# Optimization experiments

Measured on AMD Instinct MI355X. Metric: run time of the kernel, lower is better.

Reference implementation:

```python
import jax, jax.numpy as jnp
import numpy as np

D_MODEL = 1024
N_HEADS = 16
D_HEAD = D_MODEL // N_HEADS


def setup_inputs() -> dict:
    key = jax.random.key(0)
    k1, k2, k3, k4, k5 = jax.random.split(key, 5)
    B, S = 2, 2048
    scale_in = 1.0 / np.sqrt(D_MODEL)
    return {
        "x": jax.random.normal(k1, (B, S, D_MODEL), dtype=jnp.float32),
        "qkv_w": jax.random.normal(k2, (3 * D_MODEL, D_MODEL), dtype=jnp.float32) * scale_in,
        "qkv_b": jax.random.normal(k3, (3 * D_MODEL,), dtype=jnp.float32) * 0.02,
        "out_w": jax.random.normal(k4, (D_MODEL, D_MODEL), dtype=jnp.float32) * scale_in,
        "out_b": jax.random.normal(k5, (D_MODEL,), dtype=jnp.float32) * 0.02,
    }


def reference(x, qkv_w, qkv_b, out_w, out_b) -> jnp.ndarray:
    B, S, D = x.shape
    # qkv projection: torch Linear stores weight as (out, in)
    qkv = x @ qkv_w.T + qkv_b                      # [B,S,3D]
    qkv = qkv.reshape(B, S, 3, N_HEADS, D_HEAD)
    qkv = jnp.transpose(qkv, (2, 0, 3, 1, 4))      # [3,B,H,S,d]
    q, k, v = qkv[0], qkv[1], qkv[2]
    scale = 1.0 / np.sqrt(D_HEAD).astype(np.float32)
    scores = jnp.einsum("bhsd,bhtd->bhst", q, k) * scale  # [B,H,S,S]
    attn = jax.nn.softmax(scores, axis=-1)
    out = jnp.einsum("bhst,bhtd->bhsd", attn, v)   # [B,H,S,d]
    out = jnp.transpose(out, (0, 2, 1, 3)).reshape(B, S, D)
    return out @ out_w.T + out_b
```

## Files before the change

kernel.cpp:

```cpp
#include <hip/hip_runtime.h>

typedef __bf16 bf16;
typedef __bf16 bf16x4 __attribute__((ext_vector_type(4)));
typedef __bf16 bf16x8 __attribute__((ext_vector_type(8)));
typedef float  f32x4  __attribute__((ext_vector_type(4)));

__device__ __forceinline__ void gld16(const void* g, void* l) {
  __builtin_amdgcn_global_load_lds(
      (const __attribute__((address_space(1))) void*)g,
      (__attribute__((address_space(3))) void*)l, 16, 0, 0);
}

__global__ void f2bf_all(const float* __restrict__ x, bf16* __restrict__ xo,
                         const float* __restrict__ w1, bf16* __restrict__ w1o,
                         const float* __restrict__ w2, bf16* __restrict__ w2o) {
  int i = blockIdx.x * blockDim.x + threadIdx.x;
  const float* in; bf16* out; int idx;
  if (i < 1048576)      { in = x;  out = xo;  idx = i; }
  else if (i < 1835008) { in = w1; out = w1o; idx = i - 1048576; }
  else                  { in = w2; out = w2o; idx = i - 1835008; }
  float4 v = reinterpret_cast<const float4*>(in)[idx];
  bf16x4 o = { (bf16)v.x, (bf16)v.y, (bf16)v.z, (bf16)v.w };
  reinterpret_cast<bf16x4*>(out)[idx] = o;
}

template<int MODE, int BN>
__global__ __launch_bounds__(256)
void gemm_bt(const bf16* __restrict__ A, const bf16* __restrict__ B,
             const float* __restrict__ bias, void* __restrict__ Cout,
             int K, int N) {
  __shared__ bf16 As[128 * 64];
  __shared__ bf16 Bs[BN * 64];
  const int tid  = threadIdx.x;
  const int wave = tid >> 6, lane = tid & 63;
  const int quad = lane >> 4, l16 = lane & 15;
  const int bm = blockIdx.x * 128, bn = blockIdx.y * BN;
  constexpr int NI  = (BN == 128) ? 4 : 2;
  constexpr int BCH = BN / 32;
  const int wr = (BN == 128) ? (wave >> 1) * 64 : wave * 32;
  const int wc = (BN == 128) ? (wave & 1) * 64 : 0;
  const int arow = lane >> 3;
  const int acol = (lane & 7) * 8;

  f32x4 acc[NI][4] = {};

  const bf16* Ab = A + (size_t)bm * K;
  const bf16* Bb = B + (size_t)bn * K;

  for (int k0 = 0; k0 < K; k0 += 64) {
#pragma unroll
    for (int i = 0; i < 4; ++i) {
      int c = wave * 4 + i;
      gld16(Ab + (size_t)(c * 8 + arow) * K + k0 + acol, As + c * 512);
    }
#pragma unroll
    for (int i = 0; i < BCH; ++i) {
      int c = wave * BCH + i;
      gld16(Bb + (size_t)(c * 8 + arow) * K + k0 + acol, Bs + c * 512);
    }
    __syncthreads();
#pragma unroll
    for (int kk = 0; kk < 64; kk += 32) {
      bf16x8 af[NI], bfr[4];
#pragma unroll
      for (int i = 0; i < NI; ++i)
        af[i]  = *(const bf16x8*)(As + (wr + i * 16 + l16) * 64 + kk + quad * 8);
#pragma unroll
      for (int j = 0; j < 4; ++j)
        bfr[j] = *(const bf16x8*)(Bs + (wc + j * 16 + l16) * 64 + kk + quad * 8);
#pragma unroll
      for (int i = 0; i < NI; ++i)
#pragma unroll
        for (int j = 0; j < 4; ++j)
          acc[i][j] = __builtin_amdgcn_mfma_f32_16x16x32_bf16(af[i], bfr[j], acc[i][j], 0, 0, 0);
    }
    __syncthreads();
  }

  if constexpr (MODE == 0) {
    bf16* Q = (bf16*)Cout;
#pragma unroll
    for (int j = 0; j < 4; ++j) {
      int col = bn + wc + j * 16 + l16;
      float bv  = bias[col];
      int sec = col >> 10, rem = col & 1023;
      int h = rem >> 6, d = rem & 63;
      float scl = (sec == 0) ? 0.125f * 1.44269504f : 1.0f;
#pragma unroll
      for (int i = 0; i < NI; ++i) {
#pragma unroll
        for (int r = 0; r < 4; ++r) {
          int row = bm + wr + i * 16 + quad * 4 + r;
          int b = row >> 11, si = row & 2047;
          float v = (acc[i][j][r] + bv) * scl;
          Q[(((size_t)sec * 32 + b * 16 + h) * 2048 + si) * 64 + d] = (bf16)v;
        }
      }
    }
  } else {
    float* C = (float*)Cout;
#pragma unroll
    for (int j = 0; j < 4; ++j) {
      int col = bn + wc + j * 16 + l16;
      float bv = bias[col];
#pragma unroll
      for (int i = 0; i < NI; ++i)
#pragma unroll
        for (int r = 0; r < 4; ++r) {
          int row = bm + wr + i * 16 + quad * 4 + r;
          C[(size_t)row * N + col] = acc[i][j][r] + bv;
        }
    }
  }
}

__global__ __launch_bounds__(256)
void transpose_v(const bf16* __restrict__ V, bf16* __restrict__ Vt) {
  __shared__ bf16 t[64][72];
  int bh = blockIdx.y, s0 = blockIdx.x * 64;
  const bf16* Vb = V + ((size_t)bh * 2048 + s0) * 64;
  bf16* Vtb = Vt + (size_t)bh * 64 * 2048 + s0;
  int tid = threadIdx.x;
#pragma unroll
  for (int p = 0; p < 2; ++p) {
    int r = p * 32 + (tid >> 3), c0 = (tid & 7) * 8;
    bf16x8 v = *(const bf16x8*)(Vb + r * 64 + c0);
#pragma unroll
    for (int j = 0; j < 8; ++j) t[c0 + j][r] = v[j];
  }
  __syncthreads();
#pragma unroll
  for (int p = 0; p < 2; ++p) {
    int d = p * 32 + (tid >> 3), s = (tid & 7) * 8;
    *(bf16x8*)(Vtb + (size_t)d * 2048 + s) = *(const bf16x8*)(&t[d][s]);
  }
}

__global__ __launch_bounds__(256, 2)
void attn_kernel(const bf16* __restrict__ QKV, const bf16* __restrict__ Vt,
                 bf16* __restrict__ O) {
  __shared__ bf16 Ks[2][128 * 72];
  __shared__ bf16 Ps[4][32 * 136];

  const int bh = blockIdx.y;
  const int q0 = blockIdx.x * 128;
  const bf16* Qg = QKV + ((size_t)bh * 2048 + q0) * 64;
  const bf16* Kg = QKV + (size_t)32 * 2048 * 64 + (size_t)bh * 2048 * 64;
  const bf16* Vg = Vt + (size_t)bh * 64 * 2048;

  const int tid  = threadIdx.x;
  const int wave = tid >> 6, lane = tid & 63;
  const int quad = lane >> 4, l16 = lane & 15;
  const int srow = tid >> 3;
  const int scol = (tid & 7) * 8;
  bf16* Pw = &Ps[wave][0];

  bf16x8 aq[2][2];
#pragma unroll
  for (int i = 0; i < 2; ++i)
#pragma unroll
    for (int kh = 0; kh < 2; ++kh)
      aq[i][kh] = *(const bf16x8*)(Qg + (size_t)(wave * 32 + i * 16 + l16) * 64 +
                                   kh * 32 + quad * 8);

  {
    bf16x8 kreg[4];
#pragma unroll
    for (int ch = 0; ch < 4; ++ch)
      kreg[ch] = *(const bf16x8*)(Kg + (size_t)(ch * 32 + srow) * 64 + scol);
#pragma unroll
    for (int ch = 0; ch < 4; ++ch)
      *(bf16x8*)(&Ks[0][(ch * 32 + srow) * 72 + scol]) = kreg[ch];
  }
  __syncthreads();

  float rs[2] = {0.f, 0.f};
  f32x4 o[2][4] = {};

  for (int kt = 0; kt < 16; ++kt) {
    const int cur = kt & 1;

    bf16x8 kreg[4];
    if (kt < 15) {
#pragma unroll
      for (int ch = 0; ch < 4; ++ch)
        kreg[ch] = *(const bf16x8*)(Kg + (size_t)((kt + 1) * 128 + ch * 32 + srow) * 64 + scol);
    }
    bf16x8 bv[4][4];
#pragma unroll
    for (int kk = 0; kk < 4; ++kk)
#pragma unroll
      for (int oj = 0; oj < 4; ++oj)
        bv[kk][oj] = *(const bf16x8*)(Vg + (size_t)(oj * 16 + l16) * 2048 +
                                      kt * 128 + kk * 32 + quad * 8);

    f32x4 s[2][8] = {};
#pragma unroll
    for (int kh = 0; kh < 2; ++kh) {
#pragma unroll
      for (int ni = 0; ni < 8; ++ni) {
        bf16x8 bk = *(const bf16x8*)(&Ks[cur][(ni * 16 + l16) * 72 + kh * 32 + quad * 8]);
        s[0][ni] = __builtin_amdgcn_mfma_f32_16x16x32_bf16(bk, aq[0][kh], s[0][ni], 0, 0, 0);
        s[1][ni] = __builtin_amdgcn_mfma_f32_16x16x32_bf16(bk, aq[1][kh], s[1][ni], 0, 0, 0);
      }
    }

    if (kt < 15) {
#pragma unroll
      for (int ch = 0; ch < 4; ++ch)
        *(bf16x8*)(&Ks[cur ^ 1][(ch * 32 + srow) * 72 + scol]) = kreg[ch];
    }

#pragma unroll
    for (int i = 0; i < 2; ++i)
#pragma unroll
      for (int ni = 0; ni < 8; ++ni) {
        float p0 = __builtin_amdgcn_exp2f(s[i][ni][0]);
        float p1 = __builtin_amdgcn_exp2f(s[i][ni][1]);
        float p2 = __builtin_amdgcn_exp2f(s[i][ni][2]);
        float p3 = __builtin_amdgcn_exp2f(s[i][ni][3]);
        rs[i] += (p0 + p1) + (p2 + p3);
        bf16x4 pk = { (bf16)p0, (bf16)p1, (bf16)p2, (bf16)p3 };
        *(bf16x4*)(Pw + (i * 16 + l16) * 136 + ni * 16 + quad * 4) = pk;
      }

#pragma unroll
    for (int kk = 0; kk < 4; ++kk) {
#pragma unroll
      for (int i = 0; i < 2; ++i) {
        bf16x8 ap = *(const bf16x8*)(Pw + (i * 16 + l16) * 136 + kk * 32 + quad * 8);
#pragma unroll
        for (int oj = 0; oj < 4; ++oj)
          o[i][oj] = __builtin_amdgcn_mfma_f32_16x16x32_bf16(ap, bv[kk][oj], o[i][oj], 0, 0, 0);
      }
    }

    __syncthreads();
  }

#pragma unroll
  for (int i = 0; i < 2; ++i) {
    rs[i] += __shfl_xor(rs[i], 16);
    rs[i] += __shfl_xor(rs[i], 32);
  }

  const int b = bh >> 4, h = bh & 15;
#pragma unroll
  for (int i = 0; i < 2; ++i)
#pragma unroll
    for (int r = 0; r < 4; ++r) {
      float lsum = __shfl(rs[i], quad * 4 + r);
      float inv = 1.0f / lsum;
      int row = q0 + wave * 32 + i * 16 + quad * 4 + r;
#pragma unroll
      for (int oj = 0; oj < 4; ++oj)
        O[((size_t)(b * 2048 + row)) * 1024 + h * 64 + oj * 16 + l16] =
            (bf16)(o[i][oj][r] * inv);
    }
}

extern "C" void kernel_launch(void* const* d_in, const int* in_sizes, int n_in,
                              void* d_out, int out_size, void* d_ws, size_t ws_size,
                              hipStream_t stream) {
  const float* x      = (const float*)d_in[0];
  const float* qkv_w  = (const float*)d_in[1];
  const float* qkv_b  = (const float*)d_in[2];
  const float* out_w  = (const float*)d_in[3];
  const float* out_b  = (const float*)d_in[4];
  float* out = (float*)d_out;

  char* ws = (char*)d_ws;
  bf16* Xb   = (bf16*)(ws);
  bf16* Wqkv = (bf16*)(ws + 8388608);
  bf16* Wout = (bf16*)(ws + 14680064);
  bf16* QKV  = (bf16*)(ws + 16777216);
  bf16* At   = (bf16*)(ws + 41943040);
  bf16* Vt   = Xb;

  f2bf_all<<<8192, 256, 0, stream>>>(x, Xb, qkv_w, Wqkv, out_w, Wout);

  gemm_bt<0, 128><<<dim3(32, 24), 256, 0, stream>>>(Xb, Wqkv, qkv_b, (void*)QKV, 1024, 3072);

  transpose_v<<<dim3(32, 32), 256, 0, stream>>>(QKV + (size_t)2 * 32 * 2048 * 64, Vt);

  attn_kernel<<<dim3(16, 32), 256, 0, stream>>>(QKV, Vt, At);

  gemm_bt<1, 64><<<dim3(32, 16), 256, 0, stream>>>(At, Wout, out_b, (void*)out, 1024, 1024);
}
```

Before: 228.1 us.

## Halve attention query tile to 64 rows and compute row sums via MFMA

Each attention block now handles 64 query rows (16 per wave) instead of 128, doubling the grid to 1024 blocks and raising the launch-bounds occupancy hint to 3. The softmax denominator is now accumulated with an extra MFMA against a vector of ones, which replaces the per-element VALU adds and the cross-lane shuffle reduction. This is meant to improve CU fill and reduce register pressure, at the cost of loading each K/V tile twice as often per query row. The row sum is now taken from the bf16-rounded probabilities, which slightly changes numerics.

After: 290.8 us. 1.27x slower.

```diff
diff --git a/kernel.cpp b/kernel.cpp
--- a/kernel.cpp
+++ b/kernel.cpp
@@ -136,14 +136,14 @@
   }
 }
 
-__global__ __launch_bounds__(256, 2)
+__global__ __launch_bounds__(256, 3)
 void attn_kernel(const bf16* __restrict__ QKV, const bf16* __restrict__ Vt,
                  bf16* __restrict__ O) {
   __shared__ bf16 Ks[2][128 * 72];
-  __shared__ bf16 Ps[4][32 * 136];
+  __shared__ bf16 Ps[4][16 * 136];
 
   const int bh = blockIdx.y;
-  const int q0 = blockIdx.x * 128;
+  const int q0 = blockIdx.x * 64;
   const bf16* Qg = QKV + ((size_t)bh * 2048 + q0) * 64;
   const bf16* Kg = QKV + (size_t)32 * 2048 * 64 + (size_t)bh * 2048 * 64;
   const bf16* Vg = Vt + (size_t)bh * 64 * 2048;
@@ -155,13 +155,10 @@
   const int scol = (tid & 7) * 8;
   bf16* Pw = &Ps[wave][0];
 
-  bf16x8 aq[2][2];
-#pragma unroll
-  for (int i = 0; i < 2; ++i)
-#pragma unroll
-    for (int kh = 0; kh < 2; ++kh)
-      aq[i][kh] = *(const bf16x8*)(Qg + (size_t)(wave * 32 + i * 16 + l16) * 64 +
-                                   kh * 32 + quad * 8);
+  bf16x8 aq[2];
+#pragma unroll
+  for (int kh = 0; kh < 2; ++kh)
+    aq[kh] = *(const bf16x8*)(Qg + (size_t)(wave * 16 + l16) * 64 + kh * 32 + quad * 8);
 
   {
     bf16x8 kreg[4];
@@ -174,8 +171,11 @@
   }
   __syncthreads();
 
-  float rs[2] = {0.f, 0.f};
-  f32x4 o[2][4] = {};
+  const bf16 one = (bf16)1.0f;
+  const bf16x8 bone = { one, one, one, one, one, one, one, one };
+
+  f32x4 o[4] = {};
+  f32x4 lacc = {};
 
   for (int kt = 0; kt < 16; ++kt) {
     const int cur = kt & 1;
@@ -194,14 +194,13 @@
         bv[kk][oj] = *(const bf16x8*)(Vg + (size_t)(oj * 16 + l16) * 2048 +
                                       kt * 128 + kk * 32 + quad * 8);
 
-    f32x4 s[2][8] = {};
+    f32x4 s[8] = {};
 #pragma unroll
     for (int kh = 0; kh < 2; ++kh) {
 #pragma unroll
       for (int ni = 0; ni < 8; ++ni) {
         bf16x8 bk = *(const bf16x8*)(&Ks[cur][(ni * 16 + l16) * 72 + kh * 32 + quad * 8]);
-        s[0][ni] = __builtin_amdgcn_mfma_f32_16x16x32_bf16(bk, aq[0][kh], s[0][ni], 0, 0, 0);
-        s[1][ni] = __builtin_amdgcn_mfma_f32_16x16x32_bf16(bk, aq[1][kh], s[1][ni], 0, 0, 0);
+        s[ni] = __builtin_amdgcn_mfma_f32_16x16x32_bf16(bk, aq[kh], s[ni], 0, 0, 0);
       }
     }
 
@@ -212,51 +211,37 @@
     }
 
 #pragma unroll
-    for (int i = 0; i < 2; ++i)
-#pragma unroll
-      for (int ni = 0; ni < 8; ++ni) {
-        float p0 = __builtin_amdgcn_exp2f(s[i][ni][0]);
-        float p1 = __builtin_amdgcn_exp2f(s[i][ni][1]);
-        float p2 = __builtin_amdgcn_exp2f(s[i][ni][2]);
-        float p3 = __builtin_amdgcn_exp2f(s[i][ni][3]);
-        rs[i] += (p0 + p1) + (p2 + p3);
-        bf16x4 pk = { (bf16)p0, (bf16)p1, (bf16)p2, (bf16)p3 };
-        *(bf16x4*)(Pw + (i * 16 + l16) * 136 + ni * 16 + quad * 4) = pk;
-      }
+    for (int ni = 0; ni < 8; ++ni) {
+      float p0 = __builtin_amdgcn_exp2f(s[ni][0]);
+      float p1 = __builtin_amdgcn_exp2f(s[ni][1]);
+      float p2 = __builtin_amdgcn_exp2f(s[ni][2]);
+      float p3 = __builtin_amdgcn_exp2f(s[ni][3]);
+      bf16x4 pk = { (bf16)p0, (bf16)p1, (bf16)p2, (bf16)p3 };
+      *(bf16x4*)(Pw + l16 * 136 + ni * 16 + quad * 4) = pk;
+    }
 
 #pragma unroll
     for (int kk = 0; kk < 4; ++kk) {
-#pragma unroll
-      for (int i = 0; i < 2; ++i) {
-        bf16x8 ap = *(const bf16x8*)(Pw + (i * 16 + l16) * 136 + kk * 32 + quad * 8);
-#pragma unroll
-        for (int oj = 0; oj < 4; ++oj)
-          o[i][oj] = __builtin_amdgcn_mfma_f32_16x16x32_bf16(ap, bv[kk][oj], o[i][oj], 0, 0, 0);
-      }
+      bf16x8 ap = *(const bf16x8*)(Pw + l16 * 136 + kk * 32 + quad * 8);
+      lacc = __builtin_amdgcn_mfma_f32_16x16x32_bf16(ap, bone, lacc, 0, 0, 0);
+#pragma unroll
+      for (int oj = 0; oj < 4; ++oj)
+        o[oj] = __builtin_amdgcn_mfma_f32_16x16x32_bf16(ap, bv[kk][oj], o[oj], 0, 0, 0);
     }
 
     __syncthreads();
   }
 
-#pragma unroll
-  for (int i = 0; i < 2; ++i) {
-    rs[i] += __shfl_xor(rs[i], 16);
-    rs[i] += __shfl_xor(rs[i], 32);
-  }
-
   const int b = bh >> 4, h = bh & 15;
 #pragma unroll
-  for (int i = 0; i < 2; ++i)
-#pragma unroll
-    for (int r = 0; r < 4; ++r) {
-      float lsum = __shfl(rs[i], quad * 4 + r);
-      float inv = 1.0f / lsum;
-      int row = q0 + wave * 32 + i * 16 + quad * 4 + r;
-#pragma unroll
-      for (int oj = 0; oj < 4; ++oj)
-        O[((size_t)(b * 2048 + row)) * 1024 + h * 64 + oj * 16 + l16] =
-            (bf16)(o[i][oj][r] * inv);
-    }
+  for (int r = 0; r < 4; ++r) {
+    float inv = 1.0f / lacc[r];
+    int row = q0 + wave * 16 + quad * 4 + r;
+#pragma unroll
+    for (int oj = 0; oj < 4; ++oj)
+      O[((size_t)(b * 2048 + row)) * 1024 + h * 64 + oj * 16 + l16] =
+          (bf16)(o[oj][r] * inv);
+  }
 }
 
 extern "C" void kernel_launch(void* const* d_in, const int* in_sizes, int n_in,
@@ -283,7 +268,7 @@
 
   transpose_v<<<dim3(32, 32), 256, 0, stream>>>(QKV + (size_t)2 * 32 * 2048 * 64, Vt);
 
-  attn_kernel<<<dim3(16, 32), 256, 0, stream>>>(QKV, Vt, At);
+  attn_kernel<<<dim3(32, 32), 256, 0, stream>>>(QKV, Vt, At);
 
   gemm_bt<1, 64><<<dim3(32, 16), 256, 0, stream>>>(At, Wout, out_b, (void*)out, 1024, 1024);
 }
```

## Fuse V transpose into QKV GEMM epilogue and reorder attention grid

Applied to the files above, without the earlier changes.

The QKV projection epilogue now writes the V section directly in transposed [bh][d][s] layout using packed 4-element bf16 stores, so the separate transpose_v kernel and its extra read/write pass are removed. The attention kernel now reads V^T from the QKV buffer region, and its grid is swapped so consecutive blocks cover different heads rather than consecutive query tiles of the same head. The V stores from the GEMM are strided by 2048 elements across lanes, which may be less coalesced than the original layout.

New measurement: 224.3 us. No clear change (-1.7%).

```diff
diff --git a/kernel.cpp b/kernel.cpp
--- a/kernel.cpp
+++ b/kernel.cpp
@@ -85,15 +85,27 @@
       float bv  = bias[col];
       int sec = col >> 10, rem = col & 1023;
       int h = rem >> 6, d = rem & 63;
-      float scl = (sec == 0) ? 0.125f * 1.44269504f : 1.0f;
-#pragma unroll
-      for (int i = 0; i < NI; ++i) {
-#pragma unroll
-        for (int r = 0; r < 4; ++r) {
-          int row = bm + wr + i * 16 + quad * 4 + r;
-          int b = row >> 11, si = row & 2047;
-          float v = (acc[i][j][r] + bv) * scl;
-          Q[(((size_t)sec * 32 + b * 16 + h) * 2048 + si) * 64 + d] = (bf16)v;
+      if (sec < 2) {
+        float scl = (sec == 0) ? 0.125f * 1.44269504f : 1.0f;
+#pragma unroll
+        for (int i = 0; i < NI; ++i) {
+#pragma unroll
+          for (int r = 0; r < 4; ++r) {
+            int row = bm + wr + i * 16 + quad * 4 + r;
+            int b = row >> 11, si = row & 2047;
+            float v = (acc[i][j][r] + bv) * scl;
+            Q[(((size_t)sec * 32 + b * 16 + h) * 2048 + si) * 64 + d] = (bf16)v;
+          }
+        }
+      } else {
+#pragma unroll
+        for (int i = 0; i < NI; ++i) {
+          int row0 = bm + wr + i * 16 + quad * 4;
+          int b = row0 >> 11, si = row0 & 2047;
+          bf16x4 pk = { (bf16)(acc[i][j][0] + bv), (bf16)(acc[i][j][1] + bv),
+                        (bf16)(acc[i][j][2] + bv), (bf16)(acc[i][j][3] + bv) };
+          *(bf16x4*)(Q + (size_t)2 * 4194304 +
+                     ((size_t)(b * 16 + h) * 64 + d) * 2048 + si) = pk;
         }
       }
     }
@@ -111,28 +123,6 @@
           C[(size_t)row * N + col] = acc[i][j][r] + bv;
         }
     }
-  }
-}
-
-__global__ __launch_bounds__(256)
-void transpose_v(const bf16* __restrict__ V, bf16* __restrict__ Vt) {
-  __shared__ bf16 t[64][72];
-  int bh = blockIdx.y, s0 = blockIdx.x * 64;
-  const bf16* Vb = V + ((size_t)bh * 2048 + s0) * 64;
-  bf16* Vtb = Vt + (size_t)bh * 64 * 2048 + s0;
-  int tid = threadIdx.x;
-#pragma unroll
-  for (int p = 0; p < 2; ++p) {
-    int r = p * 32 + (tid >> 3), c0 = (tid & 7) * 8;
-    bf16x8 v = *(const bf16x8*)(Vb + r * 64 + c0);
-#pragma unroll
-    for (int j = 0; j < 8; ++j) t[c0 + j][r] = v[j];
-  }
-  __syncthreads();
-#pragma unroll
-  for (int p = 0; p < 2; ++p) {
-    int d = p * 32 + (tid >> 3), s = (tid & 7) * 8;
-    *(bf16x8*)(Vtb + (size_t)d * 2048 + s) = *(const bf16x8*)(&t[d][s]);
   }
 }
 
@@ -142,8 +132,8 @@
   __shared__ bf16 Ks[2][128 * 72];
   __shared__ bf16 Ps[4][32 * 136];
 
-  const int bh = blockIdx.y;
-  const int q0 = blockIdx.x * 128;
+  const int bh = blockIdx.x;
+  const int q0 = blockIdx.y * 128;
   const bf16* Qg = QKV + ((size_t)bh * 2048 + q0) * 64;
   const bf16* Kg = QKV + (size_t)32 * 2048 * 64 + (size_t)bh * 2048 * 64;
   const bf16* Vg = Vt + (size_t)bh * 64 * 2048;
@@ -275,15 +265,13 @@
   bf16* Wout = (bf16*)(ws + 14680064);
   bf16* QKV  = (bf16*)(ws + 16777216);
   bf16* At   = (bf16*)(ws + 41943040);
-  bf16* Vt   = Xb;
+  bf16* VtP  = QKV + (size_t)2 * 32 * 2048 * 64;
 
   f2bf_all<<<8192, 256, 0, stream>>>(x, Xb, qkv_w, Wqkv, out_w, Wout);
 
   gemm_bt<0, 128><<<dim3(32, 24), 256, 0, stream>>>(Xb, Wqkv, qkv_b, (void*)QKV, 1024, 3072);
 
-  transpose_v<<<dim3(32, 32), 256, 0, stream>>>(QKV + (size_t)2 * 32 * 2048 * 64, Vt);
-
-  attn_kernel<<<dim3(16, 32), 256, 0, stream>>>(QKV, Vt, At);
+  attn_kernel<<<dim3(32, 16), 256, 0, stream>>>(QKV, VtP, At);
 
   gemm_bt<1, 64><<<dim3(32, 16), 256, 0, stream>>>(At, Wout, out_b, (void*)out, 1024, 1024);
 }
```
